# Performance work log

Measured on AMD Instinct MI355X. Metric: run time of the kernel, lower is better.

The kernel has to match this reference:

```python
import jax, jax.numpy as jnp
import numpy as np

B, N, C = 2, 5000, 768
H, D = 12, 64
E = 160000
NEG_SLOPE = 0.2


def setup_inputs() -> dict:
    key = jax.random.key(0)
    ks = jax.random.split(key, 6)
    x = jax.random.normal(ks[0], (B, N, C), dtype=jnp.float32)
    W = jax.random.normal(ks[1], (C, H * D), dtype=jnp.float32) * 0.02
    att_src = jax.random.normal(ks[2], (H, D), dtype=jnp.float32) * 0.1
    att_dst = jax.random.normal(ks[3], (H, D), dtype=jnp.float32) * 0.1
    bias = jnp.zeros((H * D,), dtype=jnp.float32)
    edge_index = jax.random.randint(ks[4], (2, E), 0, N, dtype=jnp.int32)
    return {"x": x, "W": W, "att_src": att_src, "att_dst": att_dst,
            "bias": bias, "edge_index": edge_index}


def reference(x, W, att_src, att_dst, bias, edge_index):
    # Batched GATConv with shared edge_index (PyG defaults: self-loops,
    # leaky_relu(0.2), per-dst softmax, concat heads, bias).
    loops = jnp.arange(N, dtype=edge_index.dtype)
    src = jnp.concatenate([edge_index[0], loops])  # [Etot]
    dst = jnp.concatenate([edge_index[1], loops])

    h = (x @ W).reshape(B, N, H, D)                        # [B,N,H,D]
    a_src = jnp.einsum('bnhd,hd->bnh', h, att_src)         # [B,N,H]
    a_dst = jnp.einsum('bnhd,hd->bnh', h, att_dst)

    e = jax.nn.leaky_relu(a_src[:, src] + a_dst[:, dst], NEG_SLOPE)  # [B,Etot,H]
    e = jnp.moveaxis(e, 1, 0)                              # [Etot,B,H]

    # numerically stable softmax over edges grouped by destination node
    m = jax.ops.segment_max(e, dst, num_segments=N)        # [N,B,H]
    ex = jnp.exp(e - m[dst])
    denom = jax.ops.segment_sum(ex, dst, num_segments=N)   # [N,B,H]
    alpha = ex / (denom[dst] + 1e-16)                      # [Etot,B,H]

    h_src = jnp.moveaxis(h[:, src], 1, 0)                  # [Etot,B,H,D]
    msg = alpha[..., None] * h_src
    out = jax.ops.segment_sum(msg, dst, num_segments=N)    # [N,B,H,D]
    out = jnp.moveaxis(out, 0, 1).reshape(B, N, H * D) + bias
    return out
```

## Files before the change

kernel.cpp:

```cpp
#include <hip/hip_runtime.h>

#define Bv 2
#define Nv 5000
#define Cv 768
#define Hv 12
#define Dv 64
#define Ev 160000
#define ETOT (Ev + Nv)
#define HD 768
#define NEG 0.2f
#define Mv (Bv * Nv)
#define MPAD 10240
#define DEGMAX 128
#define DEGPAD 136
#define DEGW 132

typedef __bf16 bf16x8 __attribute__((ext_vector_type(8)));
typedef float f32x4 __attribute__((ext_vector_type(4)));

#define GLD16(gsrc, ldst)                                                      \
  __builtin_amdgcn_global_load_lds(                                            \
      (const __attribute__((address_space(1))) unsigned int*)(gsrc),           \
      (__attribute__((address_space(3))) unsigned int*)(ldst), 16, 0, 0)

__device__ __forceinline__ unsigned short f2b(float f) {
  unsigned u = __float_as_uint(f);
  return (unsigned short)((u + 0x7FFFu + ((u >> 16) & 1u)) >> 16);
}

#define NB_CVTX 3840
#define NB_CVTW 576
#define NB_CNT  645
__global__ __launch_bounds__(256) void k_prep(const float* __restrict__ x,
                                              unsigned short* __restrict__ xb,
                                              const float* __restrict__ W,
                                              unsigned short* __restrict__ Wt,
                                              const int* __restrict__ ei,
                                              int* __restrict__ cnt,
                                              int* __restrict__ csrp) {
  const int blk = blockIdx.x;
  const int t = threadIdx.x;
  if (blk < NB_CVTX) {
    size_t i = ((size_t)blk * 256 + t) * 8;
    unsigned short o[8];
    if (i < (size_t)Mv * Cv) {
      float4 v0 = *(const float4*)(x + i);
      float4 v1 = *(const float4*)(x + i + 4);
      o[0] = f2b(v0.x); o[1] = f2b(v0.y); o[2] = f2b(v0.z); o[3] = f2b(v0.w);
      o[4] = f2b(v1.x); o[5] = f2b(v1.y); o[6] = f2b(v1.z); o[7] = f2b(v1.w);
    } else {
      for (int j = 0; j < 8; ++j) o[j] = 0;
    }
    *(uint4*)(xb + i) = *(const uint4*)o;
  } else if (blk < NB_CVTX + NB_CVTW) {
    __shared__ float s[32][33];
    const int bw = blk - NB_CVTX;
    const int n0 = (bw % 24) * 32, k0 = (bw / 24) * 32;
    const int tx = t & 31, ty = t >> 5;
#pragma unroll
    for (int i = 0; i < 4; ++i)
      s[ty + i * 8][tx] = W[(size_t)(k0 + ty + i * 8) * HD + n0 + tx];
    __syncthreads();
#pragma unroll
    for (int i = 0; i < 4; ++i)
      Wt[(size_t)(n0 + ty + i * 8) * Cv + k0 + tx] = f2b(s[tx][ty + i * 8]);
  } else {
    const int e = (blk - NB_CVTX - NB_CVTW) * 256 + t;
    if (e < ETOT) {
      int dst = (e < Ev) ? ei[Ev + e] : (e - Ev);
      int src = (e < Ev) ? ei[e] : (e - Ev);
      int pos = atomicAdd(&cnt[dst], 1);
      csrp[dst * DEGMAX + pos] = src;
    }
  }
}

__global__ __launch_bounds__(512) void k_gemm_mfma(const unsigned short* __restrict__ A,
                                                   const unsigned short* __restrict__ Bt,
                                                   unsigned short* __restrict__ C,
                                                   const float* __restrict__ att_src,
                                                   const float* __restrict__ att_dst,
                                                   float* __restrict__ asrc,
                                                   float* __restrict__ adst) {
  __shared__ unsigned short As[256 * 64];
  __shared__ unsigned short Bs[128 * 64];
  const int l0 = blockIdx.x;
  const int xcd = l0 & 7, j = l0 >> 3;
  const int bm = (xcd + 8 * (j / 6)) * 256;
  const int bn = (j % 6) * 128;
  const int t = threadIdx.x;
  const int w = t >> 6, l = t & 63;
  const int wr = w >> 1, wc = w & 1;
  const int g = l >> 4, li = l & 15;
  f32x4 acc[4][4] = {};

  const int rs = t >> 3;
  const int sl = (t & 7) ^ (rs & 7);

  for (int k0 = 0; k0 < Cv; k0 += 64) {
#pragma unroll
    for (int i = 0; i < 4; ++i) {
      const int r = i * 64 + rs;
      GLD16(A + (size_t)(bm + r) * Cv + k0 + sl * 8, &As[t * 8 + i * 4096]);
    }
#pragma unroll
    for (int i = 0; i < 2; ++i) {
      const int r = i * 64 + rs;
      GLD16(Bt + (size_t)(bn + r) * Cv + k0 + sl * 8, &Bs[t * 8 + i * 4096]);
    }
    __syncthreads();
#pragma unroll
    for (int ks = 0; ks < 2; ++ks) {
      bf16x8 a[4], b[4];
#pragma unroll
      for (int mi = 0; mi < 4; ++mi) {
        const int row = wr * 64 + mi * 16 + li;
        const int slot = (ks * 4 + g) ^ (row & 7);
        a[mi] = *(const bf16x8*)&As[row * 64 + slot * 8];
      }
#pragma unroll
      for (int nj = 0; nj < 4; ++nj) {
        const int row = wc * 64 + nj * 16 + li;
        const int slot = (ks * 4 + g) ^ (row & 7);
        b[nj] = *(const bf16x8*)&Bs[row * 64 + slot * 8];
      }
#pragma unroll
      for (int mi = 0; mi < 4; ++mi)
#pragma unroll
        for (int nj = 0; nj < 4; ++nj)
          acc[mi][nj] = __builtin_amdgcn_mfma_f32_16x16x32_bf16(a[mi], b[nj], acc[mi][nj], 0, 0, 0);
    }
    __syncthreads();
  }
#pragma unroll
  for (int mi = 0; mi < 4; ++mi) {
#pragma unroll
    for (int nj = 0; nj < 4; ++nj) {
      const int col = bn + wc * 64 + nj * 16 + li;
#pragma unroll
      for (int r4 = 0; r4 < 4; ++r4) {
        const int row = bm + wr * 64 + mi * 16 + g * 4 + r4;
        C[(size_t)row * HD + col] = f2b(acc[mi][nj][r4]);
      }
    }
  }
  {
    const int head = (bn >> 6) + wc;
    float aS[4], aD[4];
#pragma unroll
    for (int nj = 0; nj < 4; ++nj) {
      aS[nj] = att_src[head * Dv + nj * 16 + li];
      aD[nj] = att_dst[head * Dv + nj * 16 + li];
    }
#pragma unroll
    for (int mi = 0; mi < 4; ++mi) {
#pragma unroll
      for (int r4 = 0; r4 < 4; ++r4) {
        float vs = 0.f, vd = 0.f;
#pragma unroll
        for (int nj = 0; nj < 4; ++nj) {
          const float hv = acc[mi][nj][r4];
          vs = fmaf(hv, aS[nj], vs);
          vd = fmaf(hv, aD[nj], vd);
        }
        vs += __shfl_xor(vs, 1); vd += __shfl_xor(vd, 1);
        vs += __shfl_xor(vs, 2); vd += __shfl_xor(vd, 2);
        vs += __shfl_xor(vs, 4); vd += __shfl_xor(vd, 4);
        vs += __shfl_xor(vs, 8); vd += __shfl_xor(vd, 8);
        const int row = bm + wr * 64 + mi * 16 + g * 4 + r4;
        if (li == 0 && row < Mv) {
          asrc[(size_t)row * Hv + head] = vs;
          adst[(size_t)row * Hv + head] = vd;
        }
      }
    }
  }
}

#define EDGE_FMA(c, wv)                                              \
  {                                                                  \
    acc[0] = fmaf(wv, __uint_as_float((c).x << 16), acc[0]);         \
    acc[1] = fmaf(wv, __uint_as_float((c).x & 0xFFFF0000u), acc[1]); \
    acc[2] = fmaf(wv, __uint_as_float((c).y << 16), acc[2]);         \
    acc[3] = fmaf(wv, __uint_as_float((c).y & 0xFFFF0000u), acc[3]); \
    acc[4] = fmaf(wv, __uint_as_float((c).z << 16), acc[4]);         \
    acc[5] = fmaf(wv, __uint_as_float((c).z & 0xFFFF0000u), acc[5]); \
    acc[6] = fmaf(wv, __uint_as_float((c).w << 16), acc[6]);         \
    acc[7] = fmaf(wv, __uint_as_float((c).w & 0xFFFF0000u), acc[7]); \
  }

__global__ __launch_bounds__(192) void k_agg(const unsigned short* __restrict__ h2,
                                             const int* __restrict__ cnt,
                                             const int* __restrict__ csrp,
                                             const float* __restrict__ asrc,
                                             const float* __restrict__ adst,
                                             const float* __restrict__ bias,
                                             float* __restrict__ out) {
  const int xcd = blockIdx.x & 7;
  const int idx = blockIdx.x >> 3;
  const int b = xcd >> 2;
  const int pair = (xcd & 3) * 625 + idx;
  const int n0 = pair * 2;
  const int t = threadIdx.x;
  __shared__ int s_src[2][DEGPAD];
  __shared__ float s_w[2][Hv][DEGW];
  __shared__ float s_inv[2][16];
  const int d0 = cnt[n0], d1 = cnt[n0 + 1];
  for (int i = t; i < 2 * DEGPAD; i += 192) {
    const int jn = i >= DEGPAD;
    const int ii = i - jn * DEGPAD;
    const int dd = jn ? d1 : d0;
    int sv = 0;
    if (ii < dd) sv = csrp[(n0 + jn) * DEGMAX + ii];
    s_src[jn][ii] = sv;
  }
  __syncthreads();
  {
    const int jn = t / 96, rq = t % 96;
    const int q = rq >> 5, slot = rq & 31;
    const int deg = jn ? d1 : d0;
    const int degp = (deg + 7) & ~7;
    const f32x4 adv4 = *(const f32x4*)&adst[((size_t)b * Nv + n0 + jn) * Hv + q * 4];
    f32x4 ps = {0.f, 0.f, 0.f, 0.f};
    for (int i = slot; i < deg; i += 32) {
      const int src = s_src[jn][i];
      const f32x4 as4 = *(const f32x4*)&asrc[((size_t)b * Nv + src) * Hv + q * 4];
#pragma unroll
      for (int jq = 0; jq < 4; ++jq) {
        float v = as4[jq] + adv4[jq];
        v = fmaxf(v, NEG * v);
        float ex = __expf(v);
        s_w[jn][q * 4 + jq][i] = ex;
        ps[jq] += ex;
      }
    }
    for (int i = deg + slot; i < degp; i += 32) {
#pragma unroll
      for (int jq = 0; jq < 4; ++jq) s_w[jn][q * 4 + jq][i] = 0.f;
    }
#pragma unroll
    for (int jq = 0; jq < 4; ++jq) {
      ps[jq] += __shfl_xor(ps[jq], 1);
      ps[jq] += __shfl_xor(ps[jq], 2);
      ps[jq] += __shfl_xor(ps[jq], 4);
      ps[jq] += __shfl_xor(ps[jq], 8);
      ps[jq] += __shfl_xor(ps[jq], 16);
    }
    if (slot == 0) {
      f32x4 inv;
#pragma unroll
      for (int jq = 0; jq < 4; ++jq) inv[jq] = 1.0f / (ps[jq] + 1e-16f);
      *(f32x4*)&s_inv[jn][q * 4] = inv;
    }
  }
  __syncthreads();
  const int jn = t >= 96;
  const int tl = t - jn * 96;
  const int hl = tl >> 3;
  const int degp = ((jn ? d1 : d0) + 7) & ~7;
  float acc[8] = {};
  const unsigned short* hrow = h2 + (size_t)b * Nv * HD + tl * 8;
  uint4 cA[4], cB[4];
#pragma unroll
  for (int k = 0; k < 4; ++k)
    cA[k] = *(const uint4*)(hrow + (size_t)s_src[jn][k] * HD);
  for (int base = 0; base < degp; base += 8) {
#pragma unroll
    for (int k = 0; k < 4; ++k)
      cB[k] = *(const uint4*)(hrow + (size_t)s_src[jn][base + 4 + k] * HD);
    {
      const f32x4 w4 = *(const f32x4*)&s_w[jn][hl][base];
      EDGE_FMA(cA[0], w4[0]); EDGE_FMA(cA[1], w4[1]);
      EDGE_FMA(cA[2], w4[2]); EDGE_FMA(cA[3], w4[3]);
    }
#pragma unroll
    for (int k = 0; k < 4; ++k)
      cA[k] = *(const uint4*)(hrow + (size_t)s_src[jn][base + 8 + k] * HD);
    {
      const f32x4 w4 = *(const f32x4*)&s_w[jn][hl][base + 4];
      EDGE_FMA(cB[0], w4[0]); EDGE_FMA(cB[1], w4[1]);
      EDGE_FMA(cB[2], w4[2]); EDGE_FMA(cB[3], w4[3]);
    }
  }
  const float invh = s_inv[jn][hl];
  const int od = tl * 8;
  float4 o0, o1;
  o0.x = fmaf(acc[0], invh, bias[od + 0]);
  o0.y = fmaf(acc[1], invh, bias[od + 1]);
  o0.z = fmaf(acc[2], invh, bias[od + 2]);
  o0.w = fmaf(acc[3], invh, bias[od + 3]);
  o1.x = fmaf(acc[4], invh, bias[od + 4]);
  o1.y = fmaf(acc[5], invh, bias[od + 5]);
  o1.z = fmaf(acc[6], invh, bias[od + 6]);
  o1.w = fmaf(acc[7], invh, bias[od + 7]);
  float* op = out + ((size_t)b * Nv + n0 + jn) * HD + od;
  *(float4*)op = o0;
  *(float4*)(op + 4) = o1;
}

extern "C" void kernel_launch(void* const* d_in, const int* in_sizes, int n_in,
                              void* d_out, int out_size, void* d_ws, size_t ws_size,
                              hipStream_t stream) {
  const float* x = (const float*)d_in[0];
  const float* W = (const float*)d_in[1];
  const float* att_src = (const float*)d_in[2];
  const float* att_dst = (const float*)d_in[3];
  const float* bias = (const float*)d_in[4];
  const int* ei = (const int*)d_in[5];
  float* out = (float*)d_out;

  unsigned short* h2 = (unsigned short*)d_ws;
  unsigned short* xbf = h2 + (size_t)MPAD * HD;
  unsigned short* wt = xbf + (size_t)MPAD * HD;
  float* asrc = (float*)(wt + (size_t)HD * Cv);
  float* adst = asrc + (size_t)Bv * Nv * Hv;
  int* cnt = (int*)(adst + (size_t)Bv * Nv * Hv);
  int* csrp = cnt + Nv;

  hipMemsetAsync(cnt, 0, sizeof(int) * Nv, stream);

  k_prep<<<NB_CVTX + NB_CVTW + NB_CNT, 256, 0, stream>>>(x, xbf, W, wt, ei, cnt, csrp);
  k_gemm_mfma<<<240, 512, 0, stream>>>(xbf, wt, h2, att_src, att_dst, asrc, adst);
  k_agg<<<Bv * Nv / 2, 192, 0, stream>>>(h2, cnt, csrp, asrc, adst, bias, out);
}
```

Baseline: 98.84 us.

## Double-buffer LDS tiles in MFMA GEMM to overlap loads with compute

Result: no change. 97.54 us (-1.3%).

```diff
diff --git a/kernel.cpp b/kernel.cpp
--- a/kernel.cpp
+++ b/kernel.cpp
@@ -75,6 +75,20 @@
   }
 }
 
+#define STAGE(bi, kk)                                                          \
+  {                                                                            \
+    _Pragma("unroll")                                                          \
+    for (int i = 0; i < 4; ++i) {                                              \
+      const int r = i * 64 + rs;                                               \
+      GLD16(A + (size_t)(bm + r) * Cv + (kk) + sl * 8, &As[bi][t * 8 + i * 4096]); \
+    }                                                                          \
+    _Pragma("unroll")                                                          \
+    for (int i = 0; i < 2; ++i) {                                              \
+      const int r = i * 64 + rs;                                               \
+      GLD16(Bt + (size_t)(bn + r) * Cv + (kk) + sl * 8, &Bs[bi][t * 8 + i * 4096]); \
+    }                                                                          \
+  }
+
 __global__ __launch_bounds__(512) void k_gemm_mfma(const unsigned short* __restrict__ A,
                                                    const unsigned short* __restrict__ Bt,
                                                    unsigned short* __restrict__ C,
@@ -82,8 +96,8 @@
                                                    const float* __restrict__ att_dst,
                                                    float* __restrict__ asrc,
                                                    float* __restrict__ adst) {
-  __shared__ unsigned short As[256 * 64];
-  __shared__ unsigned short Bs[128 * 64];
+  __shared__ unsigned short As[2][256 * 64];
+  __shared__ unsigned short Bs[2][128 * 64];
   const int l0 = blockIdx.x;
   const int xcd = l0 & 7, j = l0 >> 3;
   const int bm = (xcd + 8 * (j / 6)) * 256;
@@ -97,18 +111,12 @@
   const int rs = t >> 3;
   const int sl = (t & 7) ^ (rs & 7);
 
-  for (int k0 = 0; k0 < Cv; k0 += 64) {
-#pragma unroll
-    for (int i = 0; i < 4; ++i) {
-      const int r = i * 64 + rs;
-      GLD16(A + (size_t)(bm + r) * Cv + k0 + sl * 8, &As[t * 8 + i * 4096]);
-    }
-#pragma unroll
-    for (int i = 0; i < 2; ++i) {
-      const int r = i * 64 + rs;
-      GLD16(Bt + (size_t)(bn + r) * Cv + k0 + sl * 8, &Bs[t * 8 + i * 4096]);
-    }
-    __syncthreads();
+  STAGE(0, 0);
+  __syncthreads();
+  int cur = 0;
+#pragma unroll 1
+  for (int step = 0; step < Cv / 64; ++step) {
+    if (step + 1 < Cv / 64) STAGE(cur ^ 1, (step + 1) * 64);
 #pragma unroll
     for (int ks = 0; ks < 2; ++ks) {
       bf16x8 a[4], b[4];
@@ -116,13 +124,13 @@
       for (int mi = 0; mi < 4; ++mi) {
         const int row = wr * 64 + mi * 16 + li;
         const int slot = (ks * 4 + g) ^ (row & 7);
-        a[mi] = *(const bf16x8*)&As[row * 64 + slot * 8];
+        a[mi] = *(const bf16x8*)&As[cur][row * 64 + slot * 8];
       }
 #pragma unroll
       for (int nj = 0; nj < 4; ++nj) {
         const int row = wc * 64 + nj * 16 + li;
         const int slot = (ks * 4 + g) ^ (row & 7);
-        b[nj] = *(const bf16x8*)&Bs[row * 64 + slot * 8];
+        b[nj] = *(const bf16x8*)&Bs[cur][row * 64 + slot * 8];
       }
 #pragma unroll
       for (int mi = 0; mi < 4; ++mi)
@@ -131,6 +139,7 @@
           acc[mi][nj] = __builtin_amdgcn_mfma_f32_16x16x32_bf16(a[mi], b[nj], acc[mi][nj], 0, 0, 0);
     }
     __syncthreads();
+    cur ^= 1;
   }
 #pragma unroll
   for (int mi = 0; mi < 4; ++mi) {
```
